# Optimization experiments

Measured on AMD Instinct MI355X. Metric: run time of the kernel, lower is better.

Reference implementation:

```python
import jax, jax.numpy as jnp
import numpy as np

V, D, NH, HD, FF, NL, NLOOPS = 1056, 320, 5, 64, 864, 6, 8
CAP, EPS, THETA = 0.8, 1e-6, 10000.0
B, S = 8, 2048


def rmsnorm(x, w):
    return w * (x * jax.lax.rsqrt(jnp.mean(x * x, axis=-1, keepdims=True) + EPS))


def rotate_half(x):
    x1, x2 = jnp.split(x, 2, axis=-1)
    return jnp.concatenate([-x2, x1], axis=-1)


def rope_tables(seq_len):
    freqs = 1.0 / (THETA ** (jnp.arange(0, HD, 2, dtype=jnp.float32) / HD))  # [HD/2]
    t = jnp.arange(seq_len, dtype=jnp.float32)
    f = jnp.outer(t, freqs)                      # [S, HD/2]
    f = jnp.concatenate([f, f], axis=-1)         # [S, HD]
    return jnp.cos(f), jnp.sin(f)


def setup_inputs() -> dict:
    key = jax.random.key(0)
    ks = jax.random.split(key, 12)
    std = 0.02
    inp = {
        "input_ids": jax.random.randint(ks[0], (B, S), 0, V),
        "iteration": 0,
        "embedding": jax.random.normal(ks[1], (V, D), jnp.float32),
        "iter_emb": jax.random.normal(ks[2], (NLOOPS, D), jnp.float32),
        "attn_norm_w": jnp.ones((NL, D), jnp.float32),
        "Wqkv": jax.random.normal(ks[3], (NL, 3 * D, D), jnp.float32) * std,
        "wo_w": jax.random.normal(ks[4], (NL, D, D), jnp.float32) * std,
        "router_w": jax.random.normal(ks[5], (NL, D), jnp.float32) * std,
        "mlp_norm_w": jnp.ones((NL, D), jnp.float32),
        "gate_w": jax.random.normal(ks[6], (NL, FF, D), jnp.float32) * std,
        "up_w": jax.random.normal(ks[7], (NL, FF, D), jnp.float32) * std,
        "down_w": jax.random.normal(ks[8], (NL, D, FF), jnp.float32) * std,
        "final_norm_w": jnp.ones((D,), jnp.float32),
    }
    return inp


def reference(input_ids, iteration, embedding, iter_emb, attn_norm_w, Wqkv, wo_w,
              router_w, mlp_norm_w, gate_w, up_w, down_w, final_norm_w):
    batch, seq = input_ids.shape
    k = max(1, int(seq * CAP))
    cos, sin = rope_tables(seq)                 # [S, HD]
    cos4 = cos[None, :, None, :]                # [1,S,1,HD]
    sin4 = sin[None, :, None, :]

    x = embedding[input_ids]                    # [B,S,D]
    if iteration < NLOOPS:
        x = x + iter_emb[iteration][None, None, :]

    causal = jnp.tril(jnp.ones((seq, seq), dtype=bool))
    bidx = jnp.arange(batch)[:, None]           # [B,1]

    for l in range(NL):
        # --- attention block ---
        h = rmsnorm(x, attn_norm_w[l])
        qkv = (h @ Wqkv[l].T).reshape(batch, seq, 3, NH, HD)
        q, kk, v = qkv[:, :, 0], qkv[:, :, 1], qkv[:, :, 2]   # [B,S,H,HD]
        q = q * cos4 + rotate_half(q) * sin4
        kk = kk * cos4 + rotate_half(kk) * sin4
        q, kk, v = (t.transpose(0, 2, 1, 3) for t in (q, kk, v))  # [B,H,S,HD]
        scores = jnp.einsum("bhqd,bhkd->bhqk", q, kk) / np.sqrt(HD)
        scores = jnp.where(causal, scores, -jnp.inf)
        attn = jax.nn.softmax(scores, axis=-1)
        out = jnp.einsum("bhqk,bhkd->bhqd", attn, v)
        out = out.transpose(0, 2, 1, 3).reshape(batch, seq, D)
        x = x + out @ wo_w[l].T

        # --- MoD router + SwiGLU MLP on selected tokens ---
        probs = jax.nn.sigmoid(x @ router_w[l])            # [B,S]
        topk_probs, topk_idx = jax.lax.top_k(probs, k)     # [B,K]
        sel = jnp.take_along_axis(x, topk_idx[:, :, None], axis=1)  # [B,K,D]
        hs = rmsnorm(sel, mlp_norm_w[l])
        gate = jax.nn.silu(hs @ gate_w[l].T) * (hs @ up_w[l].T)
        mlp = (gate @ down_w[l].T) * topk_probs[:, :, None]         # [B,K,D]
        x = x.at[bidx, topk_idx].add(mlp)                  # unique idx: add == scatter-set+residual

    return rmsnorm(x, final_norm_w)
```

## Files before the change

kernel.cpp:

```cpp
#include <hip/hip_runtime.h>
#include <hip/hip_bf16.h>
#include <math.h>

#define VSZ 1056
#define DD 320
#define NH 5
#define HD 64
#define FF 864
#define NL 6
#define NLOOPS 8
#define BB 8
#define SL 2048
#define KK 1638
#define EPSF 1e-6f

typedef _Float16 f16x8 __attribute__((ext_vector_type(8)));
typedef _Float16 f16x4 __attribute__((ext_vector_type(4)));
typedef float floatx16 __attribute__((ext_vector_type(16)));

__device__ inline void gll16(const void* g, void* l) {
    __builtin_amdgcn_global_load_lds((const __attribute__((address_space(1))) void*)g,
                                     (__attribute__((address_space(3))) void*)l, 16, 0, 0);
}

__global__ __launch_bounds__(256) void cast4_kernel(const float* __restrict__ s,
        _Float16* __restrict__ d, int n4) {
    int i = blockIdx.x * 256 + threadIdx.x;
    if (i >= n4) return;
    float4 v = ((const float4*)s)[i];
    f16x4 o = { (_Float16)v.x, (_Float16)v.y, (_Float16)v.z, (_Float16)v.w };
    *(f16x4*)(d + (size_t)i * 4) = o;
}

__global__ __launch_bounds__(256) void embed_kernel(const int* __restrict__ ids,
        const int* __restrict__ iter, const float* __restrict__ emb,
        const float* __restrict__ iter_emb, float* __restrict__ x) {
    int i = blockIdx.x * 256 + threadIdx.x;
    int d = i % DD, bs = i / DD;
    float v = emb[(size_t)ids[bs] * DD + d];
    int it = iter[0];
    if (it < NLOOPS) v += iter_emb[it * DD + d];
    x[i] = v;
}

template<typename OT>
__global__ __launch_bounds__(256) void rmsnorm_kernel(const float* __restrict__ x,
        const float* __restrict__ w, OT* __restrict__ out, int nrows) {
    int row = blockIdx.x * 4 + (threadIdx.x >> 6);
    int lane = threadIdx.x & 63;
    if (row >= nrows) return;
    const float* xr = x + (size_t)row * DD;
    float v[5]; float ss = 0.f;
#pragma unroll
    for (int i = 0; i < 5; ++i) { v[i] = xr[lane + i * 64]; ss += v[i] * v[i]; }
#pragma unroll
    for (int o = 32; o > 0; o >>= 1) ss += __shfl_xor(ss, o);
    float r = rsqrtf(ss * (1.f / DD) + EPSF);
    OT* orow = out + (size_t)row * DD;
#pragma unroll
    for (int i = 0; i < 5; ++i) orow[lane + i * 64] = (OT)(w[lane + i * 64] * v[i] * r);
}

__global__ __launch_bounds__(256) void gather_rmsnorm_kernel(const float* __restrict__ x,
        const int* __restrict__ tkidx, const float* __restrict__ w,
        _Float16* __restrict__ out, int nrows) {
    int row = blockIdx.x * 4 + (threadIdx.x >> 6);
    int lane = threadIdx.x & 63;
    if (row >= nrows) return;
    int b = row / KK;
    int t = tkidx[row];
    const float* xr = x + ((size_t)b * SL + t) * DD;
    float v[5]; float ss = 0.f;
#pragma unroll
    for (int i = 0; i < 5; ++i) { v[i] = xr[lane + i * 64]; ss += v[i] * v[i]; }
#pragma unroll
    for (int o = 32; o > 0; o >>= 1) ss += __shfl_xor(ss, o);
    float r = rsqrtf(ss * (1.f / DD) + EPSF);
    _Float16* orow = out + (size_t)row * DD;
#pragma unroll
    for (int i = 0; i < 5; ++i) orow[lane + i * 64] = (_Float16)(w[lane + i * 64] * v[i] * r);
}

__global__ __launch_bounds__(256) void router_kernel(const float* __restrict__ x,
        const float* __restrict__ rw, float* __restrict__ probs, int nrows) {
    int row = blockIdx.x * 4 + (threadIdx.x >> 6);
    int lane = threadIdx.x & 63;
    if (row >= nrows) return;
    const float* xr = x + (size_t)row * DD;
    float ss = 0.f;
#pragma unroll
    for (int i = 0; i < 5; ++i) ss += xr[lane + i * 64] * rw[lane + i * 64];
#pragma unroll
    for (int o = 32; o > 0; o >>= 1) ss += __shfl_xor(ss, o);
    if (lane == 0) probs[row] = 1.f / (1.f + __expf(-ss));
}

__global__ __launch_bounds__(1024) void topk_kernel(const float* __restrict__ probs,
        int* __restrict__ tkidx, float* __restrict__ tkprob) {
    __shared__ int hist[256];
    __shared__ int scn[256];
    __shared__ int outc;
    __shared__ int s_digit, s_rem;
    int b = blockIdx.x, tid = threadIdx.x;
    unsigned long long k0, k1;
    {
        unsigned int f0 = __float_as_uint(probs[b * SL + tid]);
        unsigned int f1 = __float_as_uint(probs[b * SL + tid + 1024]);
        k0 = ((unsigned long long)f0 << 32) | (unsigned int)(2047 - tid);
        k1 = ((unsigned long long)f1 << 32) | (unsigned int)(2047 - (tid + 1024));
    }
    if (tid == 0) outc = 0;
    unsigned long long prefix = 0, pmask = 0;
    int target = KK;
    for (int shift = 56; shift >= 0; shift -= 8) {
        if (tid < 256) hist[tid] = 0;
        __syncthreads();
        bool a0 = (k0 & pmask) == prefix;
        bool a1 = (k1 & pmask) == prefix;
        int d0 = (int)((k0 >> shift) & 255);
        int d1 = (int)((k1 >> shift) & 255);
        if (a0) atomicAdd(&hist[d0], 1);
        if (a1) atomicAdd(&hist[d1], 1);
        __syncthreads();
        if (tid < 256) scn[tid] = hist[tid];
        __syncthreads();
#pragma unroll
        for (int st = 1; st < 256; st <<= 1) {
            int v = 0;
            if (tid < 256 && tid + st < 256) v = scn[tid + st];
            __syncthreads();
            if (tid < 256) scn[tid] += v;
            __syncthreads();
        }
        if (tid < 256 && hist[tid] > 0) {
            int S = scn[tid];
            int Sgt = S - hist[tid];
            if (Sgt < target && target <= S) { s_digit = tid; s_rem = target - Sgt; }
        }
        __syncthreads();
        int dsel = s_digit, rem = s_rem;
        bool full = (rem == hist[dsel]);
        if (a0 && (d0 > dsel || (full && d0 == dsel))) {
            int s = atomicAdd(&outc, 1);
            tkidx[b * KK + s] = 2047 - (int)(k0 & 0xffffffffu);
            tkprob[b * KK + s] = __uint_as_float((unsigned int)(k0 >> 32));
        }
        if (a1 && (d1 > dsel || (full && d1 == dsel))) {
            int s = atomicAdd(&outc, 1);
            tkidx[b * KK + s] = 2047 - (int)(k1 & 0xffffffffu);
            tkprob[b * KK + s] = __uint_as_float((unsigned int)(k1 >> 32));
        }
        if (full) break;
        target = rem;
        prefix |= ((unsigned long long)dsel) << shift;
        pmask  |= ((unsigned long long)255) << shift;
        __syncthreads();
    }
}

__global__ __launch_bounds__(256) void prep_kernel(const _Float16* __restrict__ qkv,
        _Float16* __restrict__ Qh, _Float16* __restrict__ Kt, _Float16* __restrict__ Vt) {
    __shared__ _Float16 vt[64][72];
    int tid = threadIdx.x;
    int t = blockIdx.x, h = blockIdx.y, b = blockIdx.z;
    int bh = b * NH + h;
    int c = tid >> 5;
    int slb = tid & 31;
    const float QS = 0.125f * 1.44269504088896341f;
#pragma unroll
    for (int half = 0; half < 2; ++half) {
        int sl = half * 32 + slb;
        int s = t * 64 + sl;
        size_t rbase = ((size_t)(b * SL + s) * 3) * (NH * 64) + h * 64;
        f16x8 qv = *(const f16x8*)(qkv + rbase + c * 8);
        f16x8 qp = *(const f16x8*)(qkv + rbase + (c ^ 4) * 8);
        f16x8 kv = *(const f16x8*)(qkv + rbase + NH * 64 + c * 8);
        f16x8 kp = *(const f16x8*)(qkv + rbase + NH * 64 + (c ^ 4) * 8);
        f16x8 vv = *(const f16x8*)(qkv + rbase + 2 * NH * 64 + c * 8);
        f16x8 qo, ko;
#pragma unroll
        for (int j = 0; j < 8; ++j) {
            int d = c * 8 + j;
            float freq = exp2f(-(float)(d & 31) * 0.4152410118609203f);
            float ang = (float)s * freq;
            float cc = cosf(ang), sn = sinf(ang);
            float a = (float)qv[j], p = (float)qp[j];
            float ka = (float)kv[j], kb2 = (float)kp[j];
            float qr = (d < 32) ? a * cc - p * sn : a * cc + p * sn;
            float kr = (d < 32) ? ka * cc - kb2 * sn : ka * cc + kb2 * sn;
            qo[j] = (_Float16)(qr * QS);
            ko[j] = (_Float16)kr;
        }
        *(f16x8*)(Qh + ((size_t)bh * SL + s) * 64 + c * 8) = qo;
        *(f16x8*)(Kt + (((size_t)bh * 32 + t) * 8 + c) * 512 + sl * 8) = ko;
        *(f16x8*)(&vt[sl][c * 8]) = vv;
    }
    __syncthreads();
#pragma unroll
    for (int gg = 0; gg < 2; ++gg) {
        int oo = tid * 16 + gg * 8;
        int kc = oo >> 9;
        int d = (oo >> 3) & 63;
        f16x8 vo;
#pragma unroll
        for (int j = 0; j < 8; ++j) {
            int key = (kc >> 1) * 16 + (j & 3) + 8 * (j >> 2) + 4 * (kc & 1);
            vo[j] = vt[key][d];
        }
        *(f16x8*)(Vt + (((size_t)bh * 32 + t) * 8 + kc) * 512 + d * 8) = vo;
    }
}

__global__ __launch_bounds__(256, 2) void attn_mfma(const _Float16* __restrict__ Qh,
        const _Float16* __restrict__ Kt, const _Float16* __restrict__ Vt,
        _Float16* __restrict__ attn_out) {
    __shared__ float red[4][32][32];
    __shared__ float msh[4][32];
    __shared__ float lsh[4][32];
    int tid = threadIdx.x;
    int w = tid >> 6;
    int lane = tid & 63;
    int l31 = lane & 31, h5 = lane >> 5;
    int g = blockIdx.x;
    int j = g >> 3;
    int bh = (g & 7) + 8 * (j >> 6);
    int qt = 63 - (j & 63);
    int b = bh / NH, h = bh % NH;
    int nt = (qt >> 1) + 1;
    int qw = qt * 32;
    int myq = qw + l31;

    f16x8 qf[4];
    const _Float16* qrow = Qh + ((size_t)bh * SL + myq) * 64;
#pragma unroll
    for (int kd = 0; kd < 4; ++kd) qf[kd] = *(const f16x8*)(qrow + kd * 16 + h5 * 8);

    const _Float16* Kb = Kt + (size_t)bh * 32 * 4096;
    const _Float16* Vb = Vt + (size_t)bh * 32 * 4096;

    floatx16 O0, O1;
#pragma unroll
    for (int r = 0; r < 16; ++r) { O0[r] = 0.f; O1[r] = 0.f; }
    float m = -INFINITY, l = 0.f;

    for (int t = w; t < nt; t += 4) {
        const _Float16* kb = Kb + (size_t)t * 4096;
        const _Float16* vb = Vb + (size_t)t * 4096;
        f16x8 a0[4], a1[4], v0[4], v1[4];
#pragma unroll
        for (int kd = 0; kd < 4; ++kd) {
            int off = (kd * 2 + h5) * 512 + l31 * 8;
            a0[kd] = *(const f16x8*)(kb + off);
            a1[kd] = *(const f16x8*)(kb + off + 256);
        }
#pragma unroll
        for (int kc = 0; kc < 4; ++kc) {
            int off = (kc * 2 + h5) * 512 + l31 * 8;
            v0[kc] = *(const f16x8*)(vb + off);
            v1[kc] = *(const f16x8*)(vb + off + 256);
        }
        floatx16 S0, S1;
#pragma unroll
        for (int r = 0; r < 16; ++r) { S0[r] = 0.f; S1[r] = 0.f; }
#pragma unroll
        for (int kd = 0; kd < 4; ++kd) {
            S0 = __builtin_amdgcn_mfma_f32_32x32x16_f16(a0[kd], qf[kd], S0, 0, 0, 0);
            S1 = __builtin_amdgcn_mfma_f32_32x32x16_f16(a1[kd], qf[kd], S1, 0, 0, 0);
        }
        int t0 = t * 64;
        if (t0 + 63 > qw) {
#pragma unroll
            for (int r = 0; r < 16; ++r) {
                int key = t0 + (r & 3) + 8 * (r >> 2) + 4 * h5;
                if (key > myq) S0[r] = -INFINITY;
                if (key + 32 > myq) S1[r] = -INFINITY;
            }
        }
        float tmax = S0[0];
#pragma unroll
        for (int r = 1; r < 16; ++r) tmax = fmaxf(tmax, S0[r]);
#pragma unroll
        for (int r = 0; r < 16; ++r) tmax = fmaxf(tmax, S1[r]);
        tmax = fmaxf(tmax, __shfl_xor(tmax, 32));
        if (__any(tmax > m + 8.f)) {
            float mnew = fmaxf(m, tmax);
            float alpha = exp2f(m - mnew);
            l *= alpha; O0 *= alpha; O1 *= alpha; m = mnew;
        }
        float P0[16], P1[16]; float psum = 0.f;
#pragma unroll
        for (int r = 0; r < 16; ++r) { P0[r] = exp2f(S0[r] - m); psum += P0[r]; }
#pragma unroll
        for (int r = 0; r < 16; ++r) { P1[r] = exp2f(S1[r] - m); psum += P1[r]; }
        psum += __shfl_xor(psum, 32);
        l += psum;
#pragma unroll
        for (int sub = 0; sub < 2; ++sub) {
            const float* P = sub ? P1 : P0;
#pragma unroll
            for (int kc = 0; kc < 2; ++kc) {
                auto q01 = __builtin_amdgcn_cvt_pkrtz(P[kc * 8 + 0], P[kc * 8 + 1]);
                auto q23 = __builtin_amdgcn_cvt_pkrtz(P[kc * 8 + 2], P[kc * 8 + 3]);
                auto q45 = __builtin_amdgcn_cvt_pkrtz(P[kc * 8 + 4], P[kc * 8 + 5]);
                auto q67 = __builtin_amdgcn_cvt_pkrtz(P[kc * 8 + 6], P[kc * 8 + 7]);
                f16x8 pf;
                pf[0] = (_Float16)q01[0]; pf[1] = (_Float16)q01[1];
                pf[2] = (_Float16)q23[0]; pf[3] = (_Float16)q23[1];
                pf[4] = (_Float16)q45[0]; pf[5] = (_Float16)q45[1];
                pf[6] = (_Float16)q67[0]; pf[7] = (_Float16)q67[1];
                int ksg = sub * 2 + kc;
                O0 = __builtin_amdgcn_mfma_f32_32x32x16_f16(v0[ksg], pf, O0, 0, 0, 0);
                O1 = __builtin_amdgcn_mfma_f32_32x32x16_f16(v1[ksg], pf, O1, 0, 0, 0);
            }
        }
    }
    if (h5 == 0) msh[w][l31] = m;
    __syncthreads();
    float M = fmaxf(fmaxf(msh[0][l31], msh[1][l31]), fmaxf(msh[2][l31], msh[3][l31]));
    float wgt = exp2f(m - M);
    if (h5 == 0) lsh[w][l31] = l * wgt;
#pragma unroll
    for (int r = 0; r < 16; ++r) {
        int d = (r & 3) + 8 * (r >> 2) + 4 * h5;
        red[w][d][l31] = O0[r] * wgt;
    }
    __syncthreads();
    float lsum = lsh[0][l31] + lsh[1][l31] + lsh[2][l31] + lsh[3][l31];
    float linv = 1.f / lsum;
    if (w < 2) {
        f16x8 ov;
#pragma unroll
        for (int k = 0; k < 8; ++k) {
            int d = w * 16 + h5 * 8 + k;
            ov[k] = (_Float16)((red[0][d][l31] + red[1][d][l31] +
                                red[2][d][l31] + red[3][d][l31]) * linv);
        }
        *(f16x8*)(attn_out + ((size_t)(b * SL + myq)) * DD + h * 64 + w * 16 + h5 * 8) = ov;
    }
    __syncthreads();
#pragma unroll
    for (int r = 0; r < 16; ++r) {
        int d = (r & 3) + 8 * (r >> 2) + 4 * h5;
        red[w][d][l31] = O1[r] * wgt;
    }
    __syncthreads();
    if (w >= 2) {
        f16x8 ov;
#pragma unroll
        for (int k = 0; k < 8; ++k) {
            int d = (w - 2) * 16 + h5 * 8 + k;
            ov[k] = (_Float16)((red[0][d][l31] + red[1][d][l31] +
                                red[2][d][l31] + red[3][d][l31]) * linv);
        }
        *(f16x8*)(attn_out + ((size_t)(b * SL + myq)) * DD + h * 64 + 32 + (w - 2) * 16 + h5 * 8) = ov;
    }
}

template<int MODE>
__global__ __launch_bounds__(256) void gemm_mfma(const _Float16* __restrict__ A,
        const _Float16* __restrict__ W, _Float16* __restrict__ Ch, float* __restrict__ X,
        int M, int N, int K, const int* __restrict__ sidx, const float* __restrict__ sprob) {
    __shared__ __attribute__((aligned(16))) _Float16 As[2][4096];
    __shared__ __attribute__((aligned(16))) _Float16 Ws[2][4096];
    int tid = threadIdx.x;
    int lane = tid & 63;
    int wave = tid >> 6;
    int l31 = lane & 31, h5 = lane >> 5;
    int m0 = blockIdx.y * 128, n0 = blockIdx.x * 128;
    int wm = (wave & 1) * 64, wn = (wave >> 1) * 64;

    int srow = tid & 127;
    int skc = tid >> 7;
    int arow = m0 + srow; if (arow >= M) arow = M - 1;
    int wrow = n0 + srow; if (wrow >= N) wrow = N - 1;
    const _Float16* Ag = A + (size_t)arow * K + skc * 8;
    const _Float16* Wg = W + (size_t)wrow * K + skc * 8;
    _Float16* AsD = As[0] + (size_t)(tid & ~63) * 8;
    _Float16* WsD = Ws[0] + (size_t)(tid & ~63) * 8;

    floatx16 acc[2][2];
#pragma unroll
    for (int i = 0; i < 2; ++i)
#pragma unroll
        for (int j = 0; j < 2; ++j)
#pragma unroll
            for (int r = 0; r < 16; ++r) acc[i][j][r] = 0.f;

    gll16(Ag, AsD);
    gll16(Ag + 16, AsD + 2048);
    gll16(Wg, WsD);
    gll16(Wg + 16, WsD + 2048);
    __syncthreads();

    int nk = K >> 5;
    for (int t = 0; t < nk; ++t) {
        int buf = t & 1;
        if (t + 1 < nk) {
            int k0 = (t + 1) * 32;
            int bo = (buf ^ 1) * 4096;
            gll16(Ag + k0, AsD + bo);
            gll16(Ag + k0 + 16, AsD + bo + 2048);
            gll16(Wg + k0, WsD + bo);
            gll16(Wg + k0 + 16, WsD + bo + 2048);
        }
        const _Float16* Asb = As[buf];
        const _Float16* Wsb = Ws[buf];
#pragma unroll
        for (int ks = 0; ks < 2; ++ks) {
            int kc = ks * 2 + h5;
            f16x8 a0 = *(const f16x8*)(Asb + kc * 1024 + (wm + l31) * 8);
            f16x8 a1 = *(const f16x8*)(Asb + kc * 1024 + (wm + 32 + l31) * 8);
            f16x8 b0 = *(const f16x8*)(Wsb + kc * 1024 + (wn + l31) * 8);
            f16x8 b1 = *(const f16x8*)(Wsb + kc * 1024 + (wn + 32 + l31) * 8);
            acc[0][0] = __builtin_amdgcn_mfma_f32_32x32x16_f16(a0, b0, acc[0][0], 0, 0, 0);
            acc[0][1] = __builtin_amdgcn_mfma_f32_32x32x16_f16(a0, b1, acc[0][1], 0, 0, 0);
            acc[1][0] = __builtin_amdgcn_mfma_f32_32x32x16_f16(a1, b0, acc[1][0], 0, 0, 0);
            acc[1][1] = __builtin_amdgcn_mfma_f32_32x32x16_f16(a1, b1, acc[1][1], 0, 0, 0);
        }
        __syncthreads();
    }

#pragma unroll
    for (int ti = 0; ti < 2; ++ti) {
#pragma unroll
        for (int r = 0; r < 16; ++r) {
            int mm = m0 + wm + ti * 32 + (r & 3) + 8 * (r >> 2) + 4 * h5;
            if (mm >= M) continue;
            float scale = 1.f;
            float* xrow = nullptr;
            _Float16* crow = nullptr;
            if (MODE == 2) {
                int b = mm / KK;
                scale = sprob[mm];
                xrow = X + ((size_t)(b * SL + sidx[mm])) * N;
            } else if (MODE == 1) {
                xrow = X + (size_t)mm * N;
            } else {
                crow = Ch + (size_t)mm * N;
            }
#pragma unroll
            for (int tj = 0; tj < 2; ++tj) {
                int nn = n0 + wn + tj * 32 + l31;
                if (nn >= N) continue;
                float v = acc[ti][tj][r];
                if (MODE == 0) crow[nn] = (_Float16)v;
                else if (MODE == 1) xrow[nn] += v;
                else xrow[nn] += v * scale;
            }
        }
    }
}

__global__ __launch_bounds__(256) void gemm_gateup(const _Float16* __restrict__ A,
        const _Float16* __restrict__ Wg, const _Float16* __restrict__ Wu,
        _Float16* __restrict__ Ch, int M, int N, int K) {
    __shared__ __attribute__((aligned(16))) _Float16 As[2][4096];
    __shared__ __attribute__((aligned(16))) _Float16 Wgs[2][4096];
    __shared__ __attribute__((aligned(16))) _Float16 Wus[2][4096];
    int tid = threadIdx.x;
    int lane = tid & 63;
    int wave = tid >> 6;
    int l31 = lane & 31, h5 = lane >> 5;
    int m0 = blockIdx.y * 128, n0 = blockIdx.x * 128;
    int wm = (wave & 1) * 64, wn = (wave >> 1) * 64;

    int srow = tid & 127;
    int skc = tid >> 7;
    int arow = m0 + srow; if (arow >= M) arow = M - 1;
    int wrow = n0 + srow; if (wrow >= N) wrow = N - 1;
    const _Float16* Ag  = A  + (size_t)arow * K + skc * 8;
    const _Float16* Wgg = Wg + (size_t)wrow * K + skc * 8;
    const _Float16* Wug = Wu + (size_t)wrow * K + skc * 8;
    _Float16* AsD  = As[0]  + (size_t)(tid & ~63) * 8;
    _Float16* WgsD = Wgs[0] + (size_t)(tid & ~63) * 8;
    _Float16* WusD = Wus[0] + (size_t)(tid & ~63) * 8;

    floatx16 ag[2][2], au[2][2];
#pragma unroll
    for (int i = 0; i < 2; ++i)
#pragma unroll
        for (int j = 0; j < 2; ++j)
#pragma unroll
            for (int r = 0; r < 16; ++r) { ag[i][j][r] = 0.f; au[i][j][r] = 0.f; }

    gll16(Ag, AsD);
    gll16(Ag + 16, AsD + 2048);
    gll16(Wgg, WgsD);
    gll16(Wgg + 16, WgsD + 2048);
    gll16(Wug, WusD);
    gll16(Wug + 16, WusD + 2048);
    __syncthreads();

    int nk = K >> 5;
    for (int t = 0; t < nk; ++t) {
        int buf = t & 1;
        if (t + 1 < nk) {
            int k0 = (t + 1) * 32;
            int bo = (buf ^ 1) * 4096;
            gll16(Ag + k0, AsD + bo);
            gll16(Ag + k0 + 16, AsD + bo + 2048);
            gll16(Wgg + k0, WgsD + bo);
            gll16(Wgg + k0 + 16, WgsD + bo + 2048);
            gll16(Wug + k0, WusD + bo);
            gll16(Wug + k0 + 16, WusD + bo + 2048);
        }
        const _Float16* Asb = As[buf];
        const _Float16* Wgb = Wgs[buf];
        const _Float16* Wub = Wus[buf];
#pragma unroll
        for (int ks = 0; ks < 2; ++ks) {
            int kc = ks * 2 + h5;
            f16x8 a0 = *(const f16x8*)(Asb + kc * 1024 + (wm + l31) * 8);
            f16x8 a1 = *(const f16x8*)(Asb + kc * 1024 + (wm + 32 + l31) * 8);
            f16x8 g0 = *(const f16x8*)(Wgb + kc * 1024 + (wn + l31) * 8);
            f16x8 g1f = *(const f16x8*)(Wgb + kc * 1024 + (wn + 32 + l31) * 8);
            f16x8 u0 = *(const f16x8*)(Wub + kc * 1024 + (wn + l31) * 8);
            f16x8 u1 = *(const f16x8*)(Wub + kc * 1024 + (wn + 32 + l31) * 8);
            ag[0][0] = __builtin_amdgcn_mfma_f32_32x32x16_f16(a0, g0, ag[0][0], 0, 0, 0);
            ag[0][1] = __builtin_amdgcn_mfma_f32_32x32x16_f16(a0, g1f, ag[0][1], 0, 0, 0);
            ag[1][0] = __builtin_amdgcn_mfma_f32_32x32x16_f16(a1, g0, ag[1][0], 0, 0, 0);
            ag[1][1] = __builtin_amdgcn_mfma_f32_32x32x16_f16(a1, g1f, ag[1][1], 0, 0, 0);
            au[0][0] = __builtin_amdgcn_mfma_f32_32x32x16_f16(a0, u0, au[0][0], 0, 0, 0);
            au[0][1] = __builtin_amdgcn_mfma_f32_32x32x16_f16(a0, u1, au[0][1], 0, 0, 0);
            au[1][0] = __builtin_amdgcn_mfma_f32_32x32x16_f16(a1, u0, au[1][0], 0, 0, 0);
            au[1][1] = __builtin_amdgcn_mfma_f32_32x32x16_f16(a1, u1, au[1][1], 0, 0, 0);
        }
        __syncthreads();
    }

#pragma unroll
    for (int ti = 0; ti < 2; ++ti) {
#pragma unroll
        for (int r = 0; r < 16; ++r) {
            int mm = m0 + wm + ti * 32 + (r & 3) + 8 * (r >> 2) + 4 * h5;
            if (mm >= M) continue;
            _Float16* crow = Ch + (size_t)mm * N;
#pragma unroll
            for (int tj = 0; tj < 2; ++tj) {
                int nn = n0 + wn + tj * 32 + l31;
                if (nn >= N) continue;
                float gv = ag[ti][tj][r], uv = au[ti][tj][r];
                crow[nn] = (_Float16)((gv / (1.f + __expf(-gv))) * uv);
            }
        }
    }
}

extern "C" void kernel_launch(void* const* d_in, const int* in_sizes, int n_in,
                              void* d_out, int out_size, void* d_ws, size_t ws_size,
                              hipStream_t stream) {
    const int*   ids          = (const int*)d_in[0];
    const int*   iter         = (const int*)d_in[1];
    const float* emb          = (const float*)d_in[2];
    const float* iter_emb     = (const float*)d_in[3];
    const float* attn_norm_w  = (const float*)d_in[4];
    const float* Wqkv         = (const float*)d_in[5];
    const float* wo_w         = (const float*)d_in[6];
    const float* router_w     = (const float*)d_in[7];
    const float* mlp_norm_w   = (const float*)d_in[8];
    const float* gate_w       = (const float*)d_in[9];
    const float* up_w         = (const float*)d_in[10];
    const float* down_w       = (const float*)d_in[11];
    const float* final_norm_w = (const float*)d_in[12];
    float* out = (float*)d_out;

    const size_t XN   = (size_t)BB * SL * DD;
    const size_t QKVN = (size_t)BB * SL * 3 * DD;
    const size_t HN   = (size_t)BB * NH * SL * 64;
    char* ws = (char*)d_ws;
    size_t off = 0;
    float*    x        = (float*)(ws + off);    off += XN * 4;
    _Float16* h        = (_Float16*)(ws + off); off += XN * 2;
    _Float16* attn_out = (_Float16*)(ws + off); off += XN * 2;
    float*    probs    = (float*)(ws + off);    off += (size_t)BB * SL * 4;
    int*      tkidx    = (int*)(ws + off);      off += (size_t)BB * KK * 4;
    float*    tkprob   = (float*)(ws + off);    off += (size_t)BB * KK * 4;
    off = (off + 255) & ~(size_t)255;
    _Float16* qkvh     = (_Float16*)(ws + off); off += QKVN * 2;
    _Float16* Qh       = (_Float16*)(ws + off); off += HN * 2;
    _Float16* Kh       = (_Float16*)(ws + off); off += HN * 2;
    _Float16* Vh       = (_Float16*)(ws + off); off += HN * 2;
    _Float16* WqkvH    = (_Float16*)(ws + off);
    _Float16* woH   = WqkvH + (size_t)NL * 3 * DD * DD;
    _Float16* gateH = woH   + (size_t)NL * DD * DD;
    _Float16* upH   = gateH + (size_t)NL * FF * DD;
    _Float16* downH = upH   + (size_t)NL * FF * DD;
    _Float16* g1 = qkvh;

    cast4_kernel<<<(NL * 3 * DD * DD / 4 + 255) / 256, 256, 0, stream>>>(Wqkv, WqkvH, NL * 3 * DD * DD / 4);
    cast4_kernel<<<(NL * DD * DD / 4 + 255) / 256, 256, 0, stream>>>(wo_w, woH, NL * DD * DD / 4);
    cast4_kernel<<<(NL * FF * DD / 4 + 255) / 256, 256, 0, stream>>>(gate_w, gateH, NL * FF * DD / 4);
    cast4_kernel<<<(NL * FF * DD / 4 + 255) / 256, 256, 0, stream>>>(up_w, upH, NL * FF * DD / 4);
    cast4_kernel<<<(NL * DD * FF / 4 + 255) / 256, 256, 0, stream>>>(down_w, downH, NL * DD * FF / 4);

    embed_kernel<<<20480, 256, 0, stream>>>(ids, iter, emb, iter_emb, x);

    const int M1 = BB * SL;
    const int M2 = BB * KK;
    for (int l = 0; l < NL; ++l) {
        rmsnorm_kernel<_Float16><<<4096, 256, 0, stream>>>(x, attn_norm_w + l * DD, h, M1);
        gemm_mfma<0><<<dim3(8, 128), 256, 0, stream>>>(h, WqkvH + (size_t)l * 3 * DD * DD,
                                                       qkvh, nullptr, M1, 3 * DD, DD, nullptr, nullptr);
        prep_kernel<<<dim3(SL / 64, NH, BB), 256, 0, stream>>>(qkvh, Qh, Kh, Vh);
        attn_mfma<<<BB * NH * (SL / 32), 256, 0, stream>>>(Qh, Kh, Vh, attn_out);
        gemm_mfma<1><<<dim3(3, 128), 256, 0, stream>>>(attn_out, woH + (size_t)l * DD * DD,
                                                       nullptr, x, M1, DD, DD, nullptr, nullptr);
        router_kernel<<<4096, 256, 0, stream>>>(x, router_w + l * DD, probs, M1);
        topk_kernel<<<BB, 1024, 0, stream>>>(probs, tkidx, tkprob);
        gather_rmsnorm_kernel<<<3276, 256, 0, stream>>>(x, tkidx, mlp_norm_w + l * DD, h, M2);
        gemm_gateup<<<dim3(7, 103), 256, 0, stream>>>(h, gateH + (size_t)l * FF * DD,
                                                      upH + (size_t)l * FF * DD, g1, M2, FF, DD);
        gemm_mfma<2><<<dim3(3, 103), 256, 0, stream>>>(g1, downH + (size_t)l * DD * FF,
                                                       nullptr, x, M2, DD, FF, tkidx, tkprob);
    }
    rmsnorm_kernel<float><<<4096, 256, 0, stream>>>(x, final_norm_w, out, M1);
}
```

Before: 1.785 ms.

## Shrink GEMM tiles to 64x64 and remap workgroups XCD-aware on 1D grid

All MFMA GEMMs (qkv, wo, gate/up, down) drop from 128x128 to 64x64 output tiles, with one 32x32 MFMA accumulator per wave. Launches move to a 1D grid whose block IDs are remapped so consecutive tiles land on the same XCD. The aim is to remove padding waste where N is not a multiple of 128 (960, 320, 864), raise the workgroup count for better CU fill, and improve L2 locality per XCD. In exchange each tile does less MFMA work per LDS load, so arithmetic intensity drops and operand traffic rises.

```diff
diff --git a/kernel.cpp b/kernel.cpp
--- a/kernel.cpp
+++ b/kernel.cpp
@@ -359,18 +359,24 @@
 template<int MODE>
 __global__ __launch_bounds__(256) void gemm_mfma(const _Float16* __restrict__ A,
         const _Float16* __restrict__ W, _Float16* __restrict__ Ch, float* __restrict__ X,
-        int M, int N, int K, const int* __restrict__ sidx, const float* __restrict__ sprob) {
-    __shared__ __attribute__((aligned(16))) _Float16 As[2][4096];
-    __shared__ __attribute__((aligned(16))) _Float16 Ws[2][4096];
+        int M, int N, int K, int nn_tiles, const int* __restrict__ sidx, const float* __restrict__ sprob) {
+    __shared__ __attribute__((aligned(16))) _Float16 As[2][2048];
+    __shared__ __attribute__((aligned(16))) _Float16 Ws[2][2048];
     int tid = threadIdx.x;
     int lane = tid & 63;
     int wave = tid >> 6;
     int l31 = lane & 31, h5 = lane >> 5;
-    int m0 = blockIdx.y * 128, n0 = blockIdx.x * 128;
-    int wm = (wave & 1) * 64, wn = (wave >> 1) * 64;
-
-    int srow = tid & 127;
-    int skc = tid >> 7;
+    int nwg = gridDim.x;
+    int q = nwg >> 3, r = nwg & 7;
+    int xcd = blockIdx.x & 7, idx = blockIdx.x >> 3;
+    int wgid = (xcd < r ? xcd * (q + 1) : r * (q + 1) + (xcd - r) * q) + idx;
+    int mt = wgid / nn_tiles;
+    int nt = wgid - mt * nn_tiles;
+    int m0 = mt * 64, n0 = nt * 64;
+    int wm = (wave & 1) * 32, wn = (wave >> 1) * 32;
+
+    int srow = tid & 63;
+    int skc = tid >> 6;
     int arow = m0 + srow; if (arow >= M) arow = M - 1;
     int wrow = n0 + srow; if (wrow >= N) wrow = N - 1;
     const _Float16* Ag = A + (size_t)arow * K + skc * 8;
@@ -378,18 +384,12 @@
     _Float16* AsD = As[0] + (size_t)(tid & ~63) * 8;
     _Float16* WsD = Ws[0] + (size_t)(tid & ~63) * 8;
 
-    floatx16 acc[2][2];
-#pragma unroll
-    for (int i = 0; i < 2; ++i)
-#pragma unroll
-        for (int j = 0; j < 2; ++j)
-#pragma unroll
-            for (int r = 0; r < 16; ++r) acc[i][j][r] = 0.f;
+    floatx16 acc;
+#pragma unroll
+    for (int i = 0; i < 16; ++i) acc[i] = 0.f;
 
     gll16(Ag, AsD);
-    gll16(Ag + 16, AsD + 2048);
     gll16(Wg, WsD);
-    gll16(Wg + 16, WsD + 2048);
     __syncthreads();
 
     int nk = K >> 5;
@@ -397,75 +397,60 @@
         int buf = t & 1;
         if (t + 1 < nk) {
             int k0 = (t + 1) * 32;
-            int bo = (buf ^ 1) * 4096;
+            int bo = (buf ^ 1) * 2048;
             gll16(Ag + k0, AsD + bo);
-            gll16(Ag + k0 + 16, AsD + bo + 2048);
             gll16(Wg + k0, WsD + bo);
-            gll16(Wg + k0 + 16, WsD + bo + 2048);
         }
         const _Float16* Asb = As[buf];
         const _Float16* Wsb = Ws[buf];
 #pragma unroll
         for (int ks = 0; ks < 2; ++ks) {
             int kc = ks * 2 + h5;
-            f16x8 a0 = *(const f16x8*)(Asb + kc * 1024 + (wm + l31) * 8);
-            f16x8 a1 = *(const f16x8*)(Asb + kc * 1024 + (wm + 32 + l31) * 8);
-            f16x8 b0 = *(const f16x8*)(Wsb + kc * 1024 + (wn + l31) * 8);
-            f16x8 b1 = *(const f16x8*)(Wsb + kc * 1024 + (wn + 32 + l31) * 8);
-            acc[0][0] = __builtin_amdgcn_mfma_f32_32x32x16_f16(a0, b0, acc[0][0], 0, 0, 0);
-            acc[0][1] = __builtin_amdgcn_mfma_f32_32x32x16_f16(a0, b1, acc[0][1], 0, 0, 0);
-            acc[1][0] = __builtin_amdgcn_mfma_f32_32x32x16_f16(a1, b0, acc[1][0], 0, 0, 0);
-            acc[1][1] = __builtin_amdgcn_mfma_f32_32x32x16_f16(a1, b1, acc[1][1], 0, 0, 0);
-        }
-        __syncthreads();
-    }
-
-#pragma unroll
-    for (int ti = 0; ti < 2; ++ti) {
-#pragma unroll
-        for (int r = 0; r < 16; ++r) {
-            int mm = m0 + wm + ti * 32 + (r & 3) + 8 * (r >> 2) + 4 * h5;
-            if (mm >= M) continue;
-            float scale = 1.f;
-            float* xrow = nullptr;
-            _Float16* crow = nullptr;
-            if (MODE == 2) {
-                int b = mm / KK;
-                scale = sprob[mm];
-                xrow = X + ((size_t)(b * SL + sidx[mm])) * N;
-            } else if (MODE == 1) {
-                xrow = X + (size_t)mm * N;
-            } else {
-                crow = Ch + (size_t)mm * N;
-            }
-#pragma unroll
-            for (int tj = 0; tj < 2; ++tj) {
-                int nn = n0 + wn + tj * 32 + l31;
-                if (nn >= N) continue;
-                float v = acc[ti][tj][r];
-                if (MODE == 0) crow[nn] = (_Float16)v;
-                else if (MODE == 1) xrow[nn] += v;
-                else xrow[nn] += v * scale;
-            }
+            f16x8 a = *(const f16x8*)(Asb + kc * 512 + (wm + l31) * 8);
+            f16x8 b = *(const f16x8*)(Wsb + kc * 512 + (wn + l31) * 8);
+            acc = __builtin_amdgcn_mfma_f32_32x32x16_f16(a, b, acc, 0, 0, 0);
+        }
+        __syncthreads();
+    }
+
+    int nn = n0 + wn + l31;
+#pragma unroll
+    for (int r2 = 0; r2 < 16; ++r2) {
+        int mm = m0 + wm + (r2 & 3) + 8 * (r2 >> 2) + 4 * h5;
+        if (mm >= M || nn >= N) continue;
+        float v = acc[r2];
+        if (MODE == 0) {
+            Ch[(size_t)mm * N + nn] = (_Float16)v;
+        } else if (MODE == 1) {
+            X[(size_t)mm * N + nn] += v;
+        } else {
+            int b = mm / KK;
+            X[((size_t)(b * SL + sidx[mm])) * N + nn] += v * sprob[mm];
         }
     }
 }
 
 __global__ __launch_bounds__(256) void gemm_gateup(const _Float16* __restrict__ A,
         const _Float16* __restrict__ Wg, const _Float16* __restrict__ Wu,
-        _Float16* __restrict__ Ch, int M, int N, int K) {
-    __shared__ __attribute__((aligned(16))) _Float16 As[2][4096];
-    __shared__ __attribute__((aligned(16))) _Float16 Wgs[2][4096];
-    __shared__ __attribute__((aligned(16))) _Float16 Wus[2][4096];
+        _Float16* __restrict__ Ch, int M, int N, int K, int nn_tiles) {
+    __shared__ __attribute__((aligned(16))) _Float16 As[2][2048];
+    __shared__ __attribute__((aligned(16))) _Float16 Wgs[2][2048];
+    __shared__ __attribute__((aligned(16))) _Float16 Wus[2][2048];
     int tid = threadIdx.x;
     int lane = tid & 63;
     int wave = tid >> 6;
     int l31 = lane & 31, h5 = lane >> 5;
-    int m0 = blockIdx.y * 128, n0 = blockIdx.x * 128;
-    int wm = (wave & 1) * 64, wn = (wave >> 1) * 64;
-
-    int srow = tid & 127;
-    int skc = tid >> 7;
+    int nwg = gridDim.x;
+    int q = nwg >> 3, r = nwg & 7;
+    int xcd = blockIdx.x & 7, idx = blockIdx.x >> 3;
+    int wgid = (xcd < r ? xcd * (q + 1) : r * (q + 1) + (xcd - r) * q) + idx;
+    int mt = wgid / nn_tiles;
+    int nt = wgid - mt * nn_tiles;
+    int m0 = mt * 64, n0 = nt * 64;
+    int wm = (wave & 1) * 32, wn = (wave >> 1) * 32;
+
+    int srow = tid & 63;
+    int skc = tid >> 6;
     int arow = m0 + srow; if (arow >= M) arow = M - 1;
     int wrow = n0 + srow; if (wrow >= N) wrow = N - 1;
     const _Float16* Ag  = A  + (size_t)arow * K + skc * 8;
@@ -475,20 +460,13 @@
     _Float16* WgsD = Wgs[0] + (size_t)(tid & ~63) * 8;
     _Float16* WusD = Wus[0] + (size_t)(tid & ~63) * 8;
 
-    floatx16 ag[2][2], au[2][2];
-#pragma unroll
-    for (int i = 0; i < 2; ++i)
-#pragma unroll
-        for (int j = 0; j < 2; ++j)
-#pragma unroll
-            for (int r = 0; r < 16; ++r) { ag[i][j][r] = 0.f; au[i][j][r] = 0.f; }
+    floatx16 ag, au;
+#pragma unroll
+    for (int i = 0; i < 16; ++i) { ag[i] = 0.f; au[i] = 0.f; }
 
     gll16(Ag, AsD);
-    gll16(Ag + 16, AsD + 2048);
     gll16(Wgg, WgsD);
-    gll16(Wgg + 16, WgsD + 2048);
     gll16(Wug, WusD);
-    gll16(Wug + 16, WusD + 2048);
     __syncthreads();
 
     int nk = K >> 5;
@@ -496,13 +474,10 @@
         int buf = t & 1;
         if (t + 1 < nk) {
             int k0 = (t + 1) * 32;
-            int bo = (buf ^ 1) * 4096;
+            int bo = (buf ^ 1) * 2048;
             gll16(Ag + k0, AsD + bo);
-            gll16(Ag + k0 + 16, AsD + bo + 2048);
             gll16(Wgg + k0, WgsD + bo);
-            gll16(Wgg + k0 + 16, WgsD + bo + 2048);
             gll16(Wug + k0, WusD + bo);
-            gll16(Wug + k0 + 16, WusD + bo + 2048);
         }
         const _Float16* Asb = As[buf];
         const _Float16* Wgb = Wgs[buf];
@@ -510,39 +485,22 @@
 #pragma unroll
         for (int ks = 0; ks < 2; ++ks) {
             int kc = ks * 2 + h5;
-            f16x8 a0 = *(const f16x8*)(Asb + kc * 1024 + (wm + l31) * 8);
-            f16x8 a1 = *(const f16x8*)(Asb + kc * 1024 + (wm + 32 + l31) * 8);
-            f16x8 g0 = *(const f16x8*)(Wgb + kc * 1024 + (wn + l31) * 8);
-            f16x8 g1f = *(const f16x8*)(Wgb + kc * 1024 + (wn + 32 + l31) * 8);
-            f16x8 u0 = *(const f16x8*)(Wub + kc * 1024 + (wn + l31) * 8);
-            f16x8 u1 = *(const f16x8*)(Wub + kc * 1024 + (wn + 32 + l31) * 8);
-            ag[0][0] = __builtin_amdgcn_mfma_f32_32x32x16_f16(a0, g0, ag[0][0], 0, 0, 0);
-            ag[0][1] = __builtin_amdgcn_mfma_f32_32x32x16_f16(a0, g1f, ag[0][1], 0, 0, 0);
-            ag[1][0] = __builtin_amdgcn_mfma_f32_32x32x16_f16(a1, g0, ag[1][0], 0, 0, 0);
-            ag[1][1] = __builtin_amdgcn_mfma_f32_32x32x16_f16(a1, g1f, ag[1][1], 0, 0, 0);
-            au[0][0] = __builtin_amdgcn_mfma_f32_32x32x16_f16(a0, u0, au[0][0], 0, 0, 0);
-            au[0][1] = __builtin_amdgcn_mfma_f32_32x32x16_f16(a0, u1, au[0][1], 0, 0, 0);
-            au[1][0] = __builtin_amdgcn_mfma_f32_32x32x16_f16(a1, u0, au[1][0], 0, 0, 0);
-            au[1][1] = __builtin_amdgcn_mfma_f32_32x32x16_f16(a1, u1, au[1][1], 0, 0, 0);
-        }
-        __syncthreads();
-    }
-
-#pragma unroll
-    for (int ti = 0; ti < 2; ++ti) {
-#pragma unroll
-        for (int r = 0; r < 16; ++r) {
-            int mm = m0 + wm + ti * 32 + (r & 3) + 8 * (r >> 2) + 4 * h5;
-            if (mm >= M) continue;
-            _Float16* crow = Ch + (size_t)mm * N;
-#pragma unroll
-            for (int tj = 0; tj < 2; ++tj) {
-                int nn = n0 + wn + tj * 32 + l31;
-                if (nn >= N) continue;
-                float gv = ag[ti][tj][r], uv = au[ti][tj][r];
-                crow[nn] = (_Float16)((gv / (1.f + __expf(-gv))) * uv);
-            }
-        }
+            f16x8 a  = *(const f16x8*)(Asb + kc * 512 + (wm + l31) * 8);
+            f16x8 g0 = *(const f16x8*)(Wgb + kc * 512 + (wn + l31) * 8);
+            f16x8 u0 = *(const f16x8*)(Wub + kc * 512 + (wn + l31) * 8);
+            ag = __builtin_amdgcn_mfma_f32_32x32x16_f16(a, g0, ag, 0, 0, 0);
+            au = __builtin_amdgcn_mfma_f32_32x32x16_f16(a, u0, au, 0, 0, 0);
+        }
+        __syncthreads();
+    }
+
+    int nn = n0 + wn + l31;
+#pragma unroll
+    for (int r2 = 0; r2 < 16; ++r2) {
+        int mm = m0 + wm + (r2 & 3) + 8 * (r2 >> 2) + 4 * h5;
+        if (mm >= M || nn >= N) continue;
+        float gv = ag[r2], uv = au[r2];
+        Ch[(size_t)mm * N + nn] = (_Float16)((gv / (1.f + __expf(-gv))) * uv);
     }
 }
 
@@ -597,21 +555,23 @@
 
     const int M1 = BB * SL;
     const int M2 = BB * KK;
+    const int MT1 = (M1 + 63) / 64;
+    const int MT2 = (M2 + 63) / 64;
     for (int l = 0; l < NL; ++l) {
         rmsnorm_kernel<_Float16><<<4096, 256, 0, stream>>>(x, attn_norm_w + l * DD, h, M1);
-        gemm_mfma<0><<<dim3(8, 128), 256, 0, stream>>>(h, WqkvH + (size_t)l * 3 * DD * DD,
-                                                       qkvh, nullptr, M1, 3 * DD, DD, nullptr, nullptr);
+        gemm_mfma<0><<<MT1 * 15, 256, 0, stream>>>(h, WqkvH + (size_t)l * 3 * DD * DD,
+                                                   qkvh, nullptr, M1, 3 * DD, DD, 15, nullptr, nullptr);
         prep_kernel<<<dim3(SL / 64, NH, BB), 256, 0, stream>>>(qkvh, Qh, Kh, Vh);
         attn_mfma<<<BB * NH * (SL / 32), 256, 0, stream>>>(Qh, Kh, Vh, attn_out);
-        gemm_mfma<1><<<dim3(3, 128), 256, 0, stream>>>(attn_out, woH + (size_t)l * DD * DD,
-                                                       nullptr, x, M1, DD, DD, nullptr, nullptr);
+        gemm_mfma<1><<<MT1 * 5, 256, 0, stream>>>(attn_out, woH + (size_t)l * DD * DD,
+                                                  nullptr, x, M1, DD, DD, 5, nullptr, nullptr);
         router_kernel<<<4096, 256, 0, stream>>>(x, router_w + l * DD, probs, M1);
         topk_kernel<<<BB, 1024, 0, stream>>>(probs, tkidx, tkprob);
         gather_rmsnorm_kernel<<<3276, 256, 0, stream>>>(x, tkidx, mlp_norm_w + l * DD, h, M2);
-        gemm_gateup<<<dim3(7, 103), 256, 0, stream>>>(h, gateH + (size_t)l * FF * DD,
-                                                      upH + (size_t)l * FF * DD, g1, M2, FF, DD);
-        gemm_mfma<2><<<dim3(3, 103), 256, 0, stream>>>(g1, downH + (size_t)l * DD * FF,
-                                                       nullptr, x, M2, DD, FF, tkidx, tkprob);
+        gemm_gateup<<<MT2 * 14, 256, 0, stream>>>(h, gateH + (size_t)l * FF * DD,
+                                                  upH + (size_t)l * FF * DD, g1, M2, FF, DD, 14);
+        gemm_mfma<2><<<MT2 * 5, 256, 0, stream>>>(g1, downH + (size_t)l * DD * FF,
+                                                  nullptr, x, M2, DD, FF, 5, tkidx, tkprob);
     }
     rmsnorm_kernel<float><<<4096, 256, 0, stream>>>(x, final_norm_w, out, M1);
 }
```

Measured after the change: 1.550 ms. 1.15x faster.
